# Kernel tuning notes

Hardware: AMD Instinct MI355X
Metric: run time of the kernel (lower is better)

The kernel has to match this reference:

```python
import jax, jax.numpy as jnp
import numpy as np

N = 2_000_000
NUM_IN = 9
F1, F2 = 32, 64
NUM_SEG = 100_000
EPS = 1e-5


def setup_inputs() -> dict:
    key = jax.random.key(0)
    ks = jax.random.split(key, 10)
    points = jax.random.normal(ks[0], (N, NUM_IN), dtype=jnp.float32)
    inverse_indices = jax.random.randint(ks[1], (N,), 0, NUM_SEG, dtype=jnp.int64)
    w1 = jax.random.normal(ks[2], (NUM_IN, F1), dtype=jnp.float32) / np.sqrt(NUM_IN)
    b1 = jax.random.normal(ks[3], (F1,), dtype=jnp.float32) * 0.01
    g1 = jnp.ones((F1,), jnp.float32)
    be1 = jnp.zeros((F1,), jnp.float32)
    w2 = jax.random.normal(ks[4], (F1, F2), dtype=jnp.float32) / np.sqrt(F1)
    b2 = jax.random.normal(ks[5], (F2,), dtype=jnp.float32) * 0.01
    g2 = jnp.ones((F2,), jnp.float32)
    be2 = jnp.zeros((F2,), jnp.float32)
    return {
        "points": points, "inverse_indices": inverse_indices, "num_segments": NUM_SEG,
        "w1": w1, "b1": b1, "g1": g1, "be1": be1,
        "w2": w2, "b2": b2, "g2": g2, "be2": be2,
    }


def _linear_bn_relu(x, w, b, gamma, beta):
    # Linear -> BatchNorm1d (training-mode batch stats, biased var, eps=1e-5) -> ReLU
    h = x @ w + b
    mean = h.mean(axis=0)
    var = h.var(axis=0)  # biased, matches torch BN normalization
    h = (h - mean) * jax.lax.rsqrt(var + EPS) * gamma + beta
    return jax.nn.relu(h)


def reference(points, inverse_indices, num_segments, w1, b1, g1, be1, w2, b2, g2, be2):
    feat = _linear_bn_relu(points, w1, b1, g1, be1)
    feat = _linear_bn_relu(feat, w2, b2, g2, be2)
    # scatter_max over dim 0; torch_scatter zero-initializes empty segments,
    # and post-ReLU features are >= 0, so clamp -inf (empty) to 0.
    seg = jax.ops.segment_max(feat, inverse_indices, num_segments=num_segments)
    return jnp.maximum(seg, 0.0)
```

## Files before the change

kernel.cpp:

```cpp
#include <hip/hip_runtime.h>

#define EPS 1e-5f
#define NIN 9
#define F1 32
#define F2 64
#define NMOM 45
#define ROWB 80
#define SHIFT 7
#define NSEGB 128
#define NBMAX 1024
#define BT_BIN 8192
#define WSTRIDE 68

#define WS_S    0
#define WS_M    16
#define WS_S2   64
#define WS_SS2  128
#define WS_SC1  192
#define WS_SH1  224
#define WS_W1P  256
#define WS_SC2  544
#define WS_SH2  608

typedef __attribute__((ext_vector_type(8))) short bf16x8;
typedef __attribute__((ext_vector_type(4))) float f32x4;

__device__ __forceinline__ unsigned int f2bf(float f) {
    unsigned int u = __float_as_uint(f);
    return (u + 0x7fffu + ((u >> 16) & 1u)) >> 16;
}
__device__ __forceinline__ unsigned int pack2(float lo, float hi) {
    return f2bf(lo) | (f2bf(hi) << 16);
}

__global__ __launch_bounds__(256, 4) void moments_kernel(
    const float* __restrict__ pts, const int* __restrict__ idx,
    float* __restrict__ ws, int* __restrict__ histc, int N, int nb)
{
    __shared__ int lhist[NBMAX];
    __shared__ float red[64];
    for (int t = threadIdx.x; t < nb; t += 256) lhist[t] = 0;

    float S[NIN], M[NMOM];
#pragma unroll
    for (int k = 0; k < NIN; ++k) S[k] = 0.f;
#pragma unroll
    for (int m = 0; m < NMOM; ++m) M[m] = 0.f;
    __syncthreads();

    const int stride = gridDim.x * blockDim.x;
    for (int i = blockIdx.x * blockDim.x + threadIdx.x; i < N; i += stride) {
        const float* p = pts + (size_t)i * NIN;
        atomicAdd(&lhist[idx[i] >> SHIFT], 1);
        float x[NIN];
#pragma unroll
        for (int k = 0; k < NIN; ++k) x[k] = p[k];
        int m = 0;
#pragma unroll
        for (int k = 0; k < NIN; ++k) {
            S[k] += x[k];
#pragma unroll
            for (int l = k; l < NIN; ++l) { M[m] = fmaf(x[k], x[l], M[m]); ++m; }
        }
    }
#pragma unroll
    for (int off = 32; off > 0; off >>= 1) {
#pragma unroll
        for (int k = 0; k < NIN; ++k) S[k] += __shfl_xor(S[k], off, 64);
#pragma unroll
        for (int m = 0; m < NMOM; ++m) M[m] += __shfl_xor(M[m], off, 64);
    }
    if (threadIdx.x < 64) red[threadIdx.x] = 0.f;
    __syncthreads();
    if ((threadIdx.x & 63) == 0) {
#pragma unroll
        for (int k = 0; k < NIN; ++k) atomicAdd(&red[WS_S + k], S[k]);
#pragma unroll
        for (int m = 0; m < NMOM; ++m) atomicAdd(&red[WS_M + m], M[m]);
    }
    __syncthreads();
    if (threadIdx.x < 64) atomicAdd(&ws[threadIdx.x], red[threadIdx.x]);
    for (int t = threadIdx.x; t < nb; t += 256)
        if (lhist[t] > 0) atomicAdd(&histc[t], lhist[t]);
}

__global__ void scan_coarse_kernel(const int* __restrict__ histc,
                                   int* __restrict__ offsets,
                                   int* __restrict__ cursor, int nb)
{
    __shared__ int part[256];
    const int tid = threadIdx.x;
    int v[4];
    int sum = 0;
    const int base = tid * 4;
#pragma unroll
    for (int j = 0; j < 4; ++j) {
        const int i = base + j;
        v[j] = (i < nb) ? histc[i] : 0;
        sum += v[j];
    }
    part[tid] = sum;
    __syncthreads();
    for (int d = 1; d < 256; d <<= 1) {
        int t = (tid >= d) ? part[tid - d] : 0;
        __syncthreads();
        part[tid] += t;
        __syncthreads();
    }
    int pre = part[tid] - sum;
#pragma unroll
    for (int j = 0; j < 4; ++j) {
        const int i = base + j;
        if (i < nb) { offsets[i] = pre; cursor[i] = pre; }
        pre += v[j];
    }
    if (tid == 255) offsets[nb] = part[255];
}

__global__ void finalize1_kernel(
    const float* __restrict__ w1, const float* __restrict__ b1,
    const float* __restrict__ g1, const float* __restrict__ be1,
    float* __restrict__ ws, float invN)
{
    __shared__ float sc1s[F1];
    const int j = threadIdx.x;
    if (j < F1) {
        float W[NIN];
        float P = 0.f;
#pragma unroll
        for (int k = 0; k < NIN; ++k) {
            W[k] = w1[k * F1 + j];
            P = fmaf(ws[WS_S + k], W[k], P);
        }
        float Q = 0.f;
        int m = 0;
#pragma unroll
        for (int k = 0; k < NIN; ++k) {
            Q = fmaf(ws[WS_M + m], W[k] * W[k], Q); ++m;
#pragma unroll
            for (int l = k + 1; l < NIN; ++l) {
                Q = fmaf(2.f * ws[WS_M + m], W[k] * W[l], Q); ++m;
            }
        }
        const float b = b1[j];
        const float mean = fmaf(P, invN, b);
        const float Eh2 = fmaf(fmaf(2.f * b, P, Q), invN, b * b);
        const float var = Eh2 - mean * mean;
        const float sc = g1[j] * rsqrtf(var + EPS);
        ws[WS_SC1 + j] = sc;
        ws[WS_SH1 + j] = be1[j] - mean * sc;
        sc1s[j] = sc;
    }
    __syncthreads();
    for (int m = threadIdx.x; m < NIN * F1; m += blockDim.x)
        ws[WS_W1P + m] = w1[m] * sc1s[m & (F1 - 1)];
}

__global__ void finalize2_kernel(
    const float* __restrict__ g2, const float* __restrict__ be2,
    const float* __restrict__ b2, float* __restrict__ ws, float invN, float padf)
{
    const int j = threadIdx.x;
    if (j < F2) {
        const float b = b2[j];
        const float S  = ws[WS_S2 + j]  - padf * b;
        const float SS = ws[WS_SS2 + j] - padf * b * b;
        const float mean = S * invN;
        const float var  = SS * invN - mean * mean;
        const float sc   = g2[j] * rsqrtf(var + EPS);
        ws[WS_SC2 + j] = sc;
        ws[WS_SH2 + j] = be2[j] - mean * sc;
    }
}

__device__ __forceinline__ void f1_row_bf16(
    const float* __restrict__ p, const float* __restrict__ wl,
    const float* __restrict__ sh1, unsigned int* __restrict__ pk )
{
    float x[NIN];
#pragma unroll
    for (int k = 0; k < NIN; ++k) x[k] = p[k];
#pragma unroll
    for (int fc = 0; fc < 4; ++fc) {
        float h[8];
#pragma unroll
        for (int jj = 0; jj < 8; ++jj) h[jj] = sh1[fc * 8 + jj];
#pragma unroll
        for (int k = 0; k < NIN; ++k) {
            const float xv = x[k];
#pragma unroll
            for (int jj = 0; jj < 8; ++jj)
                h[jj] = fmaf(xv, wl[k * F1 + fc * 8 + jj], h[jj]);
        }
#pragma unroll
        for (int jj = 0; jj < 4; ++jj)
            pk[fc * 4 + jj] = pack2(fmaxf(h[2 * jj], 0.f), fmaxf(h[2 * jj + 1], 0.f));
    }
}

__global__ __launch_bounds__(256, 3) void f1stats_kernel(
    const float* __restrict__ pts, const float* __restrict__ w2,
    const float* __restrict__ b2, float* __restrict__ ws,
    uint4* __restrict__ f1buf, int N)
{
    __shared__ __align__(16) unsigned char stag[4][64 * ROWB];
    __shared__ float red[2 * F2];

    const int lane = threadIdx.x & 63, wv = threadIdx.x >> 6;
    const int quad = lane >> 4, m16 = lane & 15;

    bf16x8 bfr[4];
#pragma unroll
    for (int nt = 0; nt < 4; ++nt)
#pragma unroll
        for (int j = 0; j < 8; ++j)
            bfr[nt][j] = (short)f2bf(w2[(quad * 8 + j) * F2 + nt * 16 + m16]);
    float b2f[4];
#pragma unroll
    for (int nt = 0; nt < 4; ++nt) b2f[nt] = b2[nt * 16 + m16];

    const float* wl  = ws + WS_W1P;
    const float* sh1 = ws + WS_SH1;
    const f32x4 zero = {0.f, 0.f, 0.f, 0.f};
    float s[4] = {0.f, 0.f, 0.f, 0.f}, ss[4] = {0.f, 0.f, 0.f, 0.f};

    unsigned char* myst = stag[wv];
    const int nchunks = (N + 63) / 64;
    for (int c = blockIdx.x * 4 + wv; c < nchunks; c += gridDim.x * 4) {
        const int i = c * 64 + lane;
        unsigned int pk[16];
        if (i < N) {
            f1_row_bf16(pts + (size_t)i * NIN, wl, sh1, pk);
        } else {
#pragma unroll
            for (int q = 0; q < 16; ++q) pk[q] = 0u;
        }
        uint4* wrow = (uint4*)(myst + lane * ROWB);
#pragma unroll
        for (int cidx = 0; cidx < 4; ++cidx)
            wrow[cidx] = make_uint4(pk[4*cidx+0], pk[4*cidx+1], pk[4*cidx+2], pk[4*cidx+3]);

        if (i < N) {
            uint4* dst = f1buf + (size_t)i * 4;
            dst[0] = make_uint4(pk[0],  pk[1],  pk[2],  pk[3]);
            dst[1] = make_uint4(pk[4],  pk[5],  pk[6],  pk[7]);
            dst[2] = make_uint4(pk[8],  pk[9],  pk[10], pk[11]);
            dst[3] = make_uint4(pk[12], pk[13], pk[14], pk[15]);
        }

        bf16x8 afr[4];
#pragma unroll
        for (int mt = 0; mt < 4; ++mt)
            afr[mt] = *(const bf16x8*)(myst + (mt * 16 + m16) * ROWB + quad * 16);
#pragma unroll
        for (int mt = 0; mt < 4; ++mt) {
#pragma unroll
            for (int nt = 0; nt < 4; ++nt) {
                f32x4 d = __builtin_amdgcn_mfma_f32_16x16x32_bf16(afr[mt], bfr[nt], zero, 0, 0, 0);
#pragma unroll
                for (int rr = 0; rr < 4; ++rr) {
                    const float v = d[rr] + b2f[nt];
                    s[nt] += v;
                    ss[nt] = fmaf(v, v, ss[nt]);
                }
            }
        }
    }

#pragma unroll
    for (int off = 16; off < 64; off <<= 1)
#pragma unroll
        for (int nt = 0; nt < 4; ++nt) {
            s[nt]  += __shfl_xor(s[nt], off, 64);
            ss[nt] += __shfl_xor(ss[nt], off, 64);
        }
    if (threadIdx.x < 2 * F2) red[threadIdx.x] = 0.f;
    __syncthreads();
    if (quad == 0) {
#pragma unroll
        for (int nt = 0; nt < 4; ++nt) {
            atomicAdd(&red[nt * 16 + m16], s[nt]);
            atomicAdd(&red[F2 + nt * 16 + m16], ss[nt]);
        }
    }
    __syncthreads();
    if (threadIdx.x < F2) {
        atomicAdd(&ws[WS_S2 + threadIdx.x],  red[threadIdx.x]);
        atomicAdd(&ws[WS_SS2 + threadIdx.x], red[F2 + threadIdx.x]);
    }
}

__global__ __launch_bounds__(256) void binning_kernel(
    const int* __restrict__ idx, int* __restrict__ cursor,
    int2* __restrict__ pair, int N, int nb)
{
    __shared__ int lcnt[NBMAX];
    __shared__ int runbase[NBMAX];
    const int tid = threadIdx.x;
    const int t0 = blockIdx.x * BT_BIN;
    for (int t = tid; t < nb; t += 256) lcnt[t] = 0;
    __syncthreads();
#pragma unroll 4
    for (int r = 0; r < BT_BIN / 256; ++r) {
        const int i = t0 + r * 256 + tid;
        if (i < N) atomicAdd(&lcnt[idx[i] >> SHIFT], 1);
    }
    __syncthreads();
    for (int t = tid; t < nb; t += 256) {
        const int c = lcnt[t];
        if (c > 0) runbase[t] = atomicAdd(&cursor[t], c);
        lcnt[t] = 0;
    }
    __syncthreads();
#pragma unroll 4
    for (int r = 0; r < BT_BIN / 256; ++r) {
        const int i = t0 + r * 256 + tid;
        if (i < N) {
            const int sg = idx[i];
            const int bb = sg >> SHIFT;
            const int p = runbase[bb] + atomicAdd(&lcnt[bb], 1);
            pair[p] = make_int2(i, sg);
        }
    }
}

__global__ __launch_bounds__(256, 3) void bucket_scatter_kernel(
    const uint4* __restrict__ f1buf, const int2* __restrict__ pair,
    const float* __restrict__ w2, const float* __restrict__ b2,
    const float* __restrict__ ws, const int* __restrict__ offsets,
    unsigned int* __restrict__ out, int nseg)
{
    __shared__ unsigned int win[NSEGB * WSTRIDE];
    __shared__ int2 prl[4][64];

    const int b = blockIdx.x;
    const int start = offsets[b], end = offsets[b + 1];
    const int tid = threadIdx.x;
    const int lane = tid & 63, wv = tid >> 6;
    const int quad = lane >> 4, m16 = lane & 15;

    for (int t = tid; t < NSEGB * WSTRIDE; t += 256) win[t] = 0u;

    bf16x8 bfr[4];
#pragma unroll
    for (int nt = 0; nt < 4; ++nt)
#pragma unroll
        for (int j = 0; j < 8; ++j)
            bfr[nt][j] = (short)f2bf(w2[(quad * 8 + j) * F2 + nt * 16 + m16]);
    float sc2f[4], shb[4];
#pragma unroll
    for (int nt = 0; nt < 4; ++nt) {
        const int f = nt * 16 + m16;
        sc2f[nt] = ws[WS_SC2 + f];
        shb[nt]  = fmaf(b2[f], sc2f[nt], ws[WS_SH2 + f]);
    }
    const f32x4 zero = {0.f, 0.f, 0.f, 0.f};
    __syncthreads();

    const int segbase = b << SHIFT;
    const int nch = (end - start + 63) >> 6;
    const bf16x8* fb = (const bf16x8*)f1buf;
    for (int c = wv; c < nch; c += 4) {
        const int cbase = start + c * 64;
        const int sp = cbase + lane;
        int2 pr = make_int2(0, -1);
        if (sp < end) {
            pr = pair[sp];
            pr.y -= segbase;
        }
        prl[wv][lane] = pr;

        bf16x8 afr[4];
#pragma unroll
        for (int mt = 0; mt < 4; ++mt) {
            if (cbase + mt * 16 + m16 < end) {
                const int gi = prl[wv][mt * 16 + m16].x;
                afr[mt] = fb[(size_t)gi * 4 + quad];
            } else {
#pragma unroll
                for (int j = 0; j < 8; ++j) afr[mt][j] = 0;
            }
        }
#pragma unroll
        for (int mt = 0; mt < 4; ++mt) {
            f32x4 d[4];
#pragma unroll
            for (int nt = 0; nt < 4; ++nt)
                d[nt] = __builtin_amdgcn_mfma_f32_16x16x32_bf16(afr[mt], bfr[nt], zero, 0, 0, 0);
#pragma unroll
            for (int rr = 0; rr < 4; ++rr) {
                const int sl = prl[wv][mt * 16 + quad * 4 + rr].y;
                if (sl >= 0) {
#pragma unroll
                    for (int nt = 0; nt < 4; ++nt) {
                        const float v = fmaf(d[nt][rr], sc2f[nt], shb[nt]);
                        if (v > 0.f)
                            atomicMax(&win[sl * WSTRIDE + nt * 16 + m16], __float_as_uint(v));
                    }
                }
            }
        }
    }
    __syncthreads();
    const int rows = min(NSEGB, nseg - segbase);
    for (int t = tid; t < rows * 64; t += 256)
        out[(size_t)(segbase + (t >> 6)) * 64 + (t & 63)] = win[(t >> 6) * WSTRIDE + (t & 63)];
}

__global__ __launch_bounds__(256, 3) void stats2_kernel(
    const float* __restrict__ pts, const float* __restrict__ w2,
    const float* __restrict__ b2, float* __restrict__ ws, int N)
{
    __shared__ __align__(16) unsigned char stag[4][64 * ROWB];
    __shared__ float red[2 * F2];

    const int lane = threadIdx.x & 63, wv = threadIdx.x >> 6;
    const int quad = lane >> 4, m16 = lane & 15;

    bf16x8 bfr[4];
#pragma unroll
    for (int nt = 0; nt < 4; ++nt)
#pragma unroll
        for (int j = 0; j < 8; ++j)
            bfr[nt][j] = (short)f2bf(w2[(quad * 8 + j) * F2 + nt * 16 + m16]);
    float b2f[4];
#pragma unroll
    for (int nt = 0; nt < 4; ++nt) b2f[nt] = b2[nt * 16 + m16];

    const float* wl  = ws + WS_W1P;
    const float* sh1 = ws + WS_SH1;
    const f32x4 zero = {0.f, 0.f, 0.f, 0.f};
    float s[4] = {0.f, 0.f, 0.f, 0.f}, ss[4] = {0.f, 0.f, 0.f, 0.f};

    unsigned char* myst = stag[wv];
    const int nchunks = (N + 63) / 64;
    for (int c = blockIdx.x * 4 + wv; c < nchunks; c += gridDim.x * 4) {
        const int i = c * 64 + lane;
        unsigned int pk[16];
        if (i < N) {
            f1_row_bf16(pts + (size_t)i * NIN, wl, sh1, pk);
        } else {
#pragma unroll
            for (int q = 0; q < 16; ++q) pk[q] = 0u;
        }
        uint4* wrow = (uint4*)(myst + lane * ROWB);
#pragma unroll
        for (int cidx = 0; cidx < 4; ++cidx)
            wrow[cidx] = make_uint4(pk[4*cidx+0], pk[4*cidx+1], pk[4*cidx+2], pk[4*cidx+3]);

        bf16x8 afr[4];
#pragma unroll
        for (int mt = 0; mt < 4; ++mt)
            afr[mt] = *(const bf16x8*)(myst + (mt * 16 + m16) * ROWB + quad * 16);
#pragma unroll
        for (int mt = 0; mt < 4; ++mt) {
#pragma unroll
            for (int nt = 0; nt < 4; ++nt) {
                f32x4 d = __builtin_amdgcn_mfma_f32_16x16x32_bf16(afr[mt], bfr[nt], zero, 0, 0, 0);
#pragma unroll
                for (int rr = 0; rr < 4; ++rr) {
                    const float v = d[rr] + b2f[nt];
                    s[nt] += v;
                    ss[nt] = fmaf(v, v, ss[nt]);
                }
            }
        }
    }
#pragma unroll
    for (int off = 16; off < 64; off <<= 1)
#pragma unroll
        for (int nt = 0; nt < 4; ++nt) {
            s[nt]  += __shfl_xor(s[nt], off, 64);
            ss[nt] += __shfl_xor(ss[nt], off, 64);
        }
    if (threadIdx.x < 2 * F2) red[threadIdx.x] = 0.f;
    __syncthreads();
    if (quad == 0) {
#pragma unroll
        for (int nt = 0; nt < 4; ++nt) {
            atomicAdd(&red[nt * 16 + m16], s[nt]);
            atomicAdd(&red[F2 + nt * 16 + m16], ss[nt]);
        }
    }
    __syncthreads();
    if (threadIdx.x < F2) {
        atomicAdd(&ws[WS_S2 + threadIdx.x],  red[threadIdx.x]);
        atomicAdd(&ws[WS_SS2 + threadIdx.x], red[F2 + threadIdx.x]);
    }
}

__global__ __launch_bounds__(256, 2) void bucket_scatter_gather_kernel(
    const float* __restrict__ pts, const int2* __restrict__ pair,
    const float* __restrict__ w2, const float* __restrict__ b2,
    const float* __restrict__ ws, const int* __restrict__ offsets,
    unsigned int* __restrict__ out, int nseg)
{
    __shared__ unsigned int win[NSEGB * WSTRIDE];
    __shared__ __align__(16) unsigned char stag[4][64 * ROWB];
    __shared__ int segl[4][64];

    const int b = blockIdx.x;
    const int start = offsets[b], end = offsets[b + 1];
    const int tid = threadIdx.x;
    const int lane = tid & 63, wv = tid >> 6;
    const int quad = lane >> 4, m16 = lane & 15;

    for (int t = tid; t < NSEGB * WSTRIDE; t += 256) win[t] = 0u;

    bf16x8 bfr[4];
#pragma unroll
    for (int nt = 0; nt < 4; ++nt)
#pragma unroll
        for (int j = 0; j < 8; ++j)
            bfr[nt][j] = (short)f2bf(w2[(quad * 8 + j) * F2 + nt * 16 + m16]);
    float sc2f[4], shb[4];
#pragma unroll
    for (int nt = 0; nt < 4; ++nt) {
        const int f = nt * 16 + m16;
        sc2f[nt] = ws[WS_SC2 + f];
        shb[nt]  = fmaf(b2[f], sc2f[nt], ws[WS_SH2 + f]);
    }
    const float* wl  = ws + WS_W1P;
    const float* sh1 = ws + WS_SH1;
    const f32x4 zero = {0.f, 0.f, 0.f, 0.f};
    __syncthreads();

    const int segbase = b << SHIFT;
    const int nch = (end - start + 63) >> 6;
    unsigned char* myst = stag[wv];
    for (int c = wv; c < nch; c += 4) {
        const int cbase = start + c * 64;
        const int sp = cbase + lane;
        unsigned int pk[16];
        int sl = -1;
        if (sp < end) {
            const int2 pr = pair[sp];
            f1_row_bf16(pts + (size_t)pr.x * NIN, wl, sh1, pk);
            sl = pr.y - segbase;
        } else {
#pragma unroll
            for (int q = 0; q < 16; ++q) pk[q] = 0u;
        }
        segl[wv][lane] = sl;
        uint4* wrow = (uint4*)(myst + lane * ROWB);
#pragma unroll
        for (int cidx = 0; cidx < 4; ++cidx)
            wrow[cidx] = make_uint4(pk[4*cidx+0], pk[4*cidx+1], pk[4*cidx+2], pk[4*cidx+3]);

        bf16x8 afr[4];
#pragma unroll
        for (int mt = 0; mt < 4; ++mt)
            afr[mt] = *(const bf16x8*)(myst + (mt * 16 + m16) * ROWB + quad * 16);
#pragma unroll
        for (int mt = 0; mt < 4; ++mt) {
            f32x4 d[4];
#pragma unroll
            for (int nt = 0; nt < 4; ++nt)
                d[nt] = __builtin_amdgcn_mfma_f32_16x16x32_bf16(afr[mt], bfr[nt], zero, 0, 0, 0);
#pragma unroll
            for (int rr = 0; rr < 4; ++rr) {
                const int sl2 = segl[wv][mt * 16 + quad * 4 + rr];
                if (sl2 >= 0) {
#pragma unroll
                    for (int nt = 0; nt < 4; ++nt) {
                        const float v = fmaf(d[nt][rr], sc2f[nt], shb[nt]);
                        if (v > 0.f)
                            atomicMax(&win[sl2 * WSTRIDE + nt * 16 + m16], __float_as_uint(v));
                    }
                }
            }
        }
    }
    __syncthreads();
    const int rows = min(NSEGB, nseg - segbase);
    for (int t = tid; t < rows * 64; t += 256)
        out[(size_t)(segbase + (t >> 6)) * 64 + (t & 63)] = win[(t >> 6) * WSTRIDE + (t & 63)];
}

extern "C" void kernel_launch(void* const* d_in, const int* in_sizes, int n_in,
                              void* d_out, int out_size, void* d_ws, size_t ws_size,
                              hipStream_t stream)
{
    const float* pts = (const float*)d_in[0];
    const int*   idx = (const int*)d_in[1];
    const float* w1  = (const float*)d_in[3];
    const float* b1  = (const float*)d_in[4];
    const float* g1  = (const float*)d_in[5];
    const float* be1 = (const float*)d_in[6];
    const float* w2  = (const float*)d_in[7];
    const float* b2  = (const float*)d_in[8];
    const float* g2  = (const float*)d_in[9];
    const float* be2 = (const float*)d_in[10];

    const int N = in_sizes[0] / NIN;
    const int nseg = out_size / F2;
    const int nb = (nseg + NSEGB - 1) >> SHIFT;
    const float invN = 1.0f / (float)N;
    const float padf = (float)((64 - (N & 63)) & 63);

    char* base = (char*)d_ws;
    const size_t f1bytes = (size_t)N * 64;
    const size_t pairbytes = (size_t)N * 8;
    const size_t tailbytes = 4096 + ((size_t)NBMAX + NBMAX + 1 + NBMAX) * sizeof(int) + 256;
    const size_t need_main = f1bytes + pairbytes + tailbytes;

    if (ws_size >= need_main) {
        uint4* f1buf   = (uint4*)base;
        int2*  pair    = (int2*)(base + f1bytes);
        float* ws      = (float*)(base + f1bytes + pairbytes);
        int*   histc   = (int*)(base + f1bytes + pairbytes + 4096);
        int*   offsets = histc + NBMAX;
        int*   cursor  = offsets + NBMAX + 1;

        hipMemsetAsync(ws, 0, 192 * sizeof(float), stream);
        hipMemsetAsync(histc, 0, NBMAX * sizeof(int), stream);

        moments_kernel<<<1024, 256, 0, stream>>>(pts, idx, ws, histc, N, nb);
        finalize1_kernel<<<1, 320, 0, stream>>>(w1, b1, g1, be1, ws, invN);
        scan_coarse_kernel<<<1, 256, 0, stream>>>(histc, offsets, cursor, nb);
        f1stats_kernel<<<1024, 256, 0, stream>>>(pts, w2, b2, ws, f1buf, N);
        binning_kernel<<<(N + BT_BIN - 1) / BT_BIN, 256, 0, stream>>>(
            idx, cursor, pair, N, nb);
        finalize2_kernel<<<1, 64, 0, stream>>>(g2, be2, b2, ws, invN, padf);
        bucket_scatter_kernel<<<nb, 256, 0, stream>>>(
            f1buf, pair, w2, b2, ws, offsets, (unsigned int*)d_out, nseg);
    } else {
        int2*  pair    = (int2*)base;
        float* ws      = (float*)(base + pairbytes);
        int*   histc   = (int*)(base + pairbytes + 4096);
        int*   offsets = histc + NBMAX;
        int*   cursor  = offsets + NBMAX + 1;

        hipMemsetAsync(ws, 0, 192 * sizeof(float), stream);
        hipMemsetAsync(histc, 0, NBMAX * sizeof(int), stream);

        moments_kernel<<<1024, 256, 0, stream>>>(pts, idx, ws, histc, N, nb);
        finalize1_kernel<<<1, 320, 0, stream>>>(w1, b1, g1, be1, ws, invN);
        scan_coarse_kernel<<<1, 256, 0, stream>>>(histc, offsets, cursor, nb);
        binning_kernel<<<(N + BT_BIN - 1) / BT_BIN, 256, 0, stream>>>(
            idx, cursor, pair, N, nb);
        stats2_kernel<<<1024, 256, 0, stream>>>(pts, w2, b2, ws, N);
        finalize2_kernel<<<1, 64, 0, stream>>>(g2, be2, b2, ws, invN, padf);
        bucket_scatter_gather_kernel<<<nb, 256, 0, stream>>>(
            pts, pair, w2, b2, ws, offsets, (unsigned int*)d_out, nseg);
    }
}
```

Baseline: 307.3 us.

## Fold BN2 finalize into scatter, use hardware bf16 pack, resize f1stats grid

Removes the separate finalize2 launch on the main path by computing layer-2 BN scale and shift inside bucket_scatter_kernel from the raw sums. pack2 now uses the v_cvt_pk_bf16_f32 instruction instead of software rounding. The moment accumulators become named scalars via macros so they stay in registers, and the f1stats grid is sized from the chunk count, capped at 1792. Binning now launches before f1stats; every scatter block redoes the small finalize math, and the inline asm ties the code to gfx950.

After: 313.5 us. 1.02x slower.

```diff
diff --git a/kernel.cpp b/kernel.cpp
--- a/kernel.cpp
+++ b/kernel.cpp
@@ -30,8 +30,31 @@
     return (u + 0x7fffu + ((u >> 16) & 1u)) >> 16;
 }
 __device__ __forceinline__ unsigned int pack2(float lo, float hi) {
-    return f2bf(lo) | (f2bf(hi) << 16);
-}
+    unsigned int r;
+    asm("v_cvt_pk_bf16_f32 %0, %1, %2" : "=v"(r) : "v"(lo), "v"(hi));
+    return r;
+}
+
+#define FOR_S(OP) OP(0) OP(1) OP(2) OP(3) OP(4) OP(5) OP(6) OP(7) OP(8)
+#define FOR_M(OP) \
+    OP(0,0) OP(0,1) OP(0,2) OP(0,3) OP(0,4) OP(0,5) OP(0,6) OP(0,7) OP(0,8) \
+    OP(1,1) OP(1,2) OP(1,3) OP(1,4) OP(1,5) OP(1,6) OP(1,7) OP(1,8) \
+    OP(2,2) OP(2,3) OP(2,4) OP(2,5) OP(2,6) OP(2,7) OP(2,8) \
+    OP(3,3) OP(3,4) OP(3,5) OP(3,6) OP(3,7) OP(3,8) \
+    OP(4,4) OP(4,5) OP(4,6) OP(4,7) OP(4,8) \
+    OP(5,5) OP(5,6) OP(5,7) OP(5,8) \
+    OP(6,6) OP(6,7) OP(6,8) \
+    OP(7,7) OP(7,8) \
+    OP(8,8)
+#define MIDX(k,l) ((k)*NIN - ((k)*((k)-1))/2 + ((l)-(k)))
+#define S_DECL(k)   float S_##k = 0.f;
+#define M_DECL(k,l) float M_##k##_##l = 0.f;
+#define S_ACC(k)    S_##k += x[k];
+#define M_ACC(k,l)  M_##k##_##l = fmaf(x[k], x[l], M_##k##_##l);
+#define S_RED(k)    S_##k += __shfl_xor(S_##k, off, 64);
+#define M_RED(k,l)  M_##k##_##l += __shfl_xor(M_##k##_##l, off, 64);
+#define S_ATM(k)    atomicAdd(&red[WS_S + (k)], S_##k);
+#define M_ATM(k,l)  atomicAdd(&red[WS_M + MIDX(k,l)], M_##k##_##l);
 
 __global__ __launch_bounds__(256, 4) void moments_kernel(
     const float* __restrict__ pts, const int* __restrict__ idx,
@@ -41,11 +64,8 @@
     __shared__ float red[64];
     for (int t = threadIdx.x; t < nb; t += 256) lhist[t] = 0;
 
-    float S[NIN], M[NMOM];
-#pragma unroll
-    for (int k = 0; k < NIN; ++k) S[k] = 0.f;
-#pragma unroll
-    for (int m = 0; m < NMOM; ++m) M[m] = 0.f;
+    FOR_S(S_DECL)
+    FOR_M(M_DECL)
     __syncthreads();
 
     const int stride = gridDim.x * blockDim.x;
@@ -55,28 +75,19 @@
         float x[NIN];
 #pragma unroll
         for (int k = 0; k < NIN; ++k) x[k] = p[k];
-        int m = 0;
-#pragma unroll
-        for (int k = 0; k < NIN; ++k) {
-            S[k] += x[k];
-#pragma unroll
-            for (int l = k; l < NIN; ++l) { M[m] = fmaf(x[k], x[l], M[m]); ++m; }
-        }
+        FOR_S(S_ACC)
+        FOR_M(M_ACC)
     }
 #pragma unroll
     for (int off = 32; off > 0; off >>= 1) {
-#pragma unroll
-        for (int k = 0; k < NIN; ++k) S[k] += __shfl_xor(S[k], off, 64);
-#pragma unroll
-        for (int m = 0; m < NMOM; ++m) M[m] += __shfl_xor(M[m], off, 64);
+        FOR_S(S_RED)
+        FOR_M(M_RED)
     }
     if (threadIdx.x < 64) red[threadIdx.x] = 0.f;
     __syncthreads();
     if ((threadIdx.x & 63) == 0) {
-#pragma unroll
-        for (int k = 0; k < NIN; ++k) atomicAdd(&red[WS_S + k], S[k]);
-#pragma unroll
-        for (int m = 0; m < NMOM; ++m) atomicAdd(&red[WS_M + m], M[m]);
+        FOR_S(S_ATM)
+        FOR_M(M_ATM)
     }
     __syncthreads();
     if (threadIdx.x < 64) atomicAdd(&ws[threadIdx.x], red[threadIdx.x]);
@@ -290,7 +301,7 @@
     }
 }
 
-__global__ __launch_bounds__(256) void binning_kernel(
+__global__ __launch_bounds__(256) void binning_pair_kernel(
     const int* __restrict__ idx, int* __restrict__ cursor,
     int2* __restrict__ pair, int N, int nb)
 {
@@ -327,8 +338,9 @@
 __global__ __launch_bounds__(256, 3) void bucket_scatter_kernel(
     const uint4* __restrict__ f1buf, const int2* __restrict__ pair,
     const float* __restrict__ w2, const float* __restrict__ b2,
+    const float* __restrict__ g2, const float* __restrict__ be2,
     const float* __restrict__ ws, const int* __restrict__ offsets,
-    unsigned int* __restrict__ out, int nseg)
+    unsigned int* __restrict__ out, int nseg, float invN, float padf)
 {
     __shared__ unsigned int win[NSEGB * WSTRIDE];
     __shared__ int2 prl[4][64];
@@ -351,8 +363,14 @@
 #pragma unroll
     for (int nt = 0; nt < 4; ++nt) {
         const int f = nt * 16 + m16;
-        sc2f[nt] = ws[WS_SC2 + f];
-        shb[nt]  = fmaf(b2[f], sc2f[nt], ws[WS_SH2 + f]);
+        const float bb2 = b2[f];
+        const float Sv  = ws[WS_S2 + f]  - padf * bb2;
+        const float SSv = ws[WS_SS2 + f] - padf * bb2 * bb2;
+        const float mean = Sv * invN;
+        const float var  = SSv * invN - mean * mean;
+        const float sc   = g2[f] * rsqrtf(var + EPS);
+        sc2f[nt] = sc;
+        shb[nt]  = fmaf(bb2, sc, be2[f] - mean * sc);
     }
     const f32x4 zero = {0.f, 0.f, 0.f, 0.f};
     __syncthreads();
@@ -604,6 +622,11 @@
     const size_t tailbytes = 4096 + ((size_t)NBMAX + NBMAX + 1 + NBMAX) * sizeof(int) + 256;
     const size_t need_main = f1bytes + pairbytes + tailbytes;
 
+    const int nch = (N + 63) / 64;
+    int f1grid = (nch + 19) / 20;
+    if (f1grid > 1792) f1grid = 1792;
+    if (f1grid < 1) f1grid = 1;
+
     if (ws_size >= need_main) {
         uint4* f1buf   = (uint4*)base;
         int2*  pair    = (int2*)(base + f1bytes);
@@ -618,12 +641,12 @@
         moments_kernel<<<1024, 256, 0, stream>>>(pts, idx, ws, histc, N, nb);
         finalize1_kernel<<<1, 320, 0, stream>>>(w1, b1, g1, be1, ws, invN);
         scan_coarse_kernel<<<1, 256, 0, stream>>>(histc, offsets, cursor, nb);
-        f1stats_kernel<<<1024, 256, 0, stream>>>(pts, w2, b2, ws, f1buf, N);
-        binning_kernel<<<(N + BT_BIN - 1) / BT_BIN, 256, 0, stream>>>(
+        binning_pair_kernel<<<(N + BT_BIN - 1) / BT_BIN, 256, 0, stream>>>(
             idx, cursor, pair, N, nb);
-        finalize2_kernel<<<1, 64, 0, stream>>>(g2, be2, b2, ws, invN, padf);
+        f1stats_kernel<<<f1grid, 256, 0, stream>>>(pts, w2, b2, ws, f1buf, N);
         bucket_scatter_kernel<<<nb, 256, 0, stream>>>(
-            f1buf, pair, w2, b2, ws, offsets, (unsigned int*)d_out, nseg);
+            f1buf, pair, w2, b2, g2, be2, ws, offsets, (unsigned int*)d_out,
+            nseg, invN, padf);
     } else {
         int2*  pair    = (int2*)base;
         float* ws      = (float*)(base + pairbytes);
@@ -637,7 +660,7 @@
         moments_kernel<<<1024, 256, 0, stream>>>(pts, idx, ws, histc, N, nb);
         finalize1_kernel<<<1, 320, 0, stream>>>(w1, b1, g1, be1, ws, invN);
         scan_coarse_kernel<<<1, 256, 0, stream>>>(histc, offsets, cursor, nb);
-        binning_kernel<<<(N + BT_BIN - 1) / BT_BIN, 256, 0, stream>>>(
+        binning_pair_kernel<<<(N + BT_BIN - 1) / BT_BIN, 256, 0, stream>>>(
             idx, cursor, pair, N, nb);
         stats2_kernel<<<1024, 256, 0, stream>>>(pts, w2, b2, ws, N);
         finalize2_kernel<<<1, 64, 0, stream>>>(g2, be2, b2, ws, invN, padf);
```
